# Kernel optimization log

Hardware: AMD Instinct MI355X
Metric: run time of the kernel (lower is better)

The kernel has to match this reference:

```python
import jax, jax.numpy as jnp
import numpy as np

N_SAMPLES = 2 ** 15          # 32768
STEP = 256                   # transform_step_size
WIN = 2048                   # transform/synthesis window
N_FRAMES = N_SAMPLES // STEP # 128
N_COEFFS = WIN // 2 + 1      # 1025
DILATIONS = (1, 2, 4, 8, 16, 32, 64, 1)


def hann(n):
    return 0.5 - 0.5 * jnp.cos(2.0 * jnp.pi * jnp.arange(n, dtype=jnp.float32) / n)


def transform(audio):
    # audio: (B, 1, N) -> magnitude STFT (B, 1024, 128)
    x = audio[:, 0, :]
    x = jnp.pad(x, ((0, 0), (0, WIN - STEP)))  # pad so n_frames == N_SAMPLES // STEP
    idx = np.arange(N_FRAMES)[:, None] * STEP + np.arange(WIN)[None, :]
    frames = x[:, idx] * hann(WIN)
    spec = jnp.abs(jnp.fft.rfft(frames, norm='ortho'))   # (B, F, 1025)
    return spec[..., : N_COEFFS - 1].transpose(0, 2, 1)  # (B, 1024, F)


def conv1x1(x, w, b):
    # x: (B, I, T), w: (O, I, 1), b: (O,)
    return jnp.einsum('oi,bit->bot', w[:, :, 0], x) + b[None, :, None]


def anticausal_block(x, w, b, dilation):
    # kernel_size=2 anti-causal dilated conv: looks at t and t+dilation (pad future)
    x_fut = jnp.pad(x, ((0, 0), (0, 0), (0, dilation)))[:, :, dilation:]
    y = (jnp.einsum('oi,bit->bot', w[:, :, 0], x)
         + jnp.einsum('oi,bit->bot', w[:, :, 1], x_fut)
         + b[None, :, None])
    y = jax.nn.leaky_relu(y, 0.2)
    y = y + x
    # do_norm: per-example max-norm
    y = y / (jnp.max(jnp.abs(y), axis=(1, 2), keepdims=True) + 1e-8)
    return y


def upsample_with_holes(x, desired_size):
    # zero-stuffing upsample: out[..., ::step] = x
    b, c, t = x.shape
    step = desired_size // t
    out = jnp.zeros((b, c, desired_size), x.dtype)
    return out.at[:, :, ::step].set(x)


def freq_domain_resonance(coeffs):
    # coeffs: (1, C, 1025) in [0, 1); per-frame decay = repeated spectral multiply
    c = jnp.clip(coeffs, 0.0, 0.9999)
    exps = jnp.arange(1, N_FRAMES + 1, dtype=coeffs.dtype)
    mags = c[:, :, None, :] ** exps[None, None, :, None]     # (1, C, F, 1025)
    frames = jnp.fft.irfft(mags, n=WIN) * hann(WIN)
    hop = WIN // 2
    total = hop * (N_FRAMES - 1) + WIN
    idx = np.arange(N_FRAMES)[:, None] * hop + np.arange(WIN)[None, :]
    out = jnp.zeros(frames.shape[:2] + (total,), frames.dtype)
    out = out.at[:, :, idx].add(frames)                      # overlap-add
    return out[..., :N_SAMPLES]                              # (1, C, N)


def fft_convolve(a, b):
    # circular-free conv via zero-padding to 2N, keep first N (matches repo fft_convolve)
    n = a.shape[-1]
    spec = jnp.fft.rfft(a, n=2 * n) * jnp.fft.rfft(b, n=2 * n)
    return jnp.fft.irfft(spec, n=2 * n)[..., :n]


def reference(audio, proj_in_w, proj_in_b, blocks_w, blocks_b,
              proj_sparse_w, proj_sparse_b, proj_dense_w, proj_dense_b, resonances):
    spec = transform(audio)                         # (B, 1024, 128)
    h = conv1x1(spec, proj_in_w, proj_in_b)         # (B, 32, 128)
    acc = jnp.zeros_like(h)
    for i, d in enumerate(DILATIONS):               # fixed 8-block stack
        h = anticausal_block(h, blocks_w[i], blocks_b[i], d)
        acc = acc + h
    x = conv1x1(acc, proj_sparse_w, proj_sparse_b)  # (B, 256, 128)
    sparse = jax.nn.relu(x)
    x = conv1x1(sparse, proj_dense_w, proj_dense_b) # (B, 32, 128)
    x = upsample_with_holes(x, N_SAMPLES)           # (B, 32, 32768)
    res = freq_domain_resonance(resonances)         # (1, 32, 32768), broadcast over B
    y = fft_convolve(x, res)                        # (B, 32, 32768)
    y = jnp.sum(y, axis=1, keepdims=True)           # (B, 1, 32768)
    return y, sparse


def setup_inputs() -> dict:
    key = jax.random.key(0)
    ks = jax.random.split(key, 12)
    u = lambda k, shape: jax.random.uniform(k, shape, jnp.float32, -0.05, 0.05)
    return {
        'audio': jax.random.normal(ks[0], (32, 1, N_SAMPLES), jnp.float32),
        'proj_in_w': u(ks[1], (32, 1024, 1)),
        'proj_in_b': jnp.zeros((32,), jnp.float32),
        'blocks_w': u(ks[2], (8, 32, 32, 2)),
        'blocks_b': jnp.zeros((8, 32), jnp.float32),
        'proj_sparse_w': u(ks[3], (256, 32, 1)),
        'proj_sparse_b': jnp.zeros((256,), jnp.float32),
        'proj_dense_w': u(ks[4], (32, 256, 1)),
        'proj_dense_b': jnp.zeros((32,), jnp.float32),
        'resonances': jax.random.uniform(ks[5], (1, 32, N_COEFFS), jnp.float32, 0.0, 1.0),
    }
```

## Files before the change

kernel.cpp:

```cpp
#include <hip/hip_runtime.h>

#define PI_F 3.14159265358979323846f

typedef short bf16x8 __attribute__((ext_vector_type(8)));
typedef float f32x4 __attribute__((ext_vector_type(4)));

#define MFMA16(acc, a, b) \
  acc = __builtin_amdgcn_mfma_f32_16x16x32_bf16(a, b, acc, 0, 0, 0)

#define WS_SPEC   0u
#define WS_H0     4194304u
#define WS_ACC    4325376u
#define WS_V      4456448u
#define WS_WTIN   4587520u
#define WS_WST    4620288u
#define WS_WDT    4628480u
#define WS_FRAMES 4636672u
#define WS_RES    6733824u

__device__ __forceinline__ void fft2048_stages(float2* buf, int tid) {
  for (int stage = 0; stage < 11; ++stage) {
    int half = 1 << stage;
    float base = -PI_F / (float)half;
    for (int t = tid; t < 1024; t += 256) {
      int j  = t & (half - 1);
      int i0 = ((t >> stage) << (stage + 1)) + j;
      int i1 = i0 + half;
      float s, c;
      __sincosf(base * (float)j, &s, &c);
      float2 u = buf[i0];
      float2 w = buf[i1];
      float tr = c * w.x - s * w.y;
      float ti = c * w.y + s * w.x;
      buf[i0] = make_float2(u.x + tr, u.y + ti);
      buf[i1] = make_float2(u.x - tr, u.y - ti);
    }
    __syncthreads();
  }
}

__global__ __launch_bounds__(256) void k_fft(const float* __restrict__ audio,
                                             const float* __restrict__ resin,
                                             float* __restrict__ spec,
                                             float* __restrict__ frames) {
  __shared__ float2 buf[2048];
  int blk = blockIdx.x;
  if (blk < 2048) {
    int b  = blk >> 6;
    int f0 = (blk & 63) * 2;
    for (int j = threadIdx.x; j < 2048; j += 256) {
      float h = 0.5f - 0.5f * __cosf(0.0030679615757712823f * (float)j);
      int i1 = f0 * 256 + j;
      int i2 = i1 + 256;
      float a1 = (i1 < 32768) ? audio[b * 32768 + i1] : 0.f;
      float a2 = (i2 < 32768) ? audio[b * 32768 + i2] : 0.f;
      buf[__brev((unsigned)j) >> 21] = make_float2(a1 * h, a2 * h);
    }
    __syncthreads();
    fft2048_stages(buf, threadIdx.x);
    const float scale = 0.5f * 0.022097086912079608f;
    for (int k = threadIdx.x; k < 1024; k += 256) {
      float2 zk = buf[k];
      float2 zn = buf[(2048 - k) & 2047];
      float f1r = zk.x + zn.x, f1i = zk.y - zn.y;
      float f2r = zk.y + zn.y, f2i = zk.x - zn.x;
      spec[(b * 128 + f0) * 1024 + k]     = sqrtf(f1r * f1r + f1i * f1i) * scale;
      spec[(b * 128 + f0 + 1) * 1024 + k] = sqrtf(f2r * f2r + f2i * f2i) * scale;
    }
  } else {
    int r = blk - 2048;
    int c = r >> 4;
    int g = r & 15;
    float e1 = (float)(2 * g + 1);
    for (int k = threadIdx.x; k < 2048; k += 256) {
      int kk = (k <= 1024) ? k : 2048 - k;
      float cv = resin[c * 1025 + kk];
      cv = fminf(fmaxf(cv, 0.f), 0.9999f);
      float m1 = __powf(cv, e1);
      float m2 = m1 * cv;
      buf[__brev((unsigned)k) >> 21] = make_float2(m1, m2);
    }
    __syncthreads();
    fft2048_stages(buf, threadIdx.x);
    for (int j = threadIdx.x; j < 2048; j += 256) {
      float h  = 0.5f - 0.5f * __cosf(0.0030679615757712823f * (float)j);
      float sc = h * (1.f / 2048.f);
      float2 z = buf[j];
      frames[(c * 32 + 2 * g) * 2048 + j]     = z.x * sc;
      frames[(c * 32 + 2 * g + 1) * 2048 + j] = z.y * sc;
    }
  }
}

__global__ __launch_bounds__(256) void k_prep(const float* __restrict__ Win,
                                              const float* __restrict__ Ws,
                                              const float* __restrict__ Wd,
                                              const float* __restrict__ bwIn,
                                              float* __restrict__ WT,
                                              float* __restrict__ WsT,
                                              float* __restrict__ WdT,
                                              short* __restrict__ Whg,
                                              short* __restrict__ Wlg) {
  int i = blockIdx.x * 256 + threadIdx.x;
  if (i < 32768) { int o = i >> 10, k = i & 1023; WT[k * 32 + o] = Win[i]; }
  if (i < 8192)  { int o2 = i >> 5, m = i & 31;   WsT[m * 256 + o2] = Ws[i]; }
  if (i < 8192)  { int c = i >> 8, o2 = i & 255;  WdT[o2 * 32 + c] = Wd[i]; }
  if (i < 16384) {
    int w = i & 1, m = (i >> 1) & 31, o = (i >> 6) & 31, s = i >> 11;
    float val = bwIn[i];
    unsigned bits = __float_as_uint(val);
    float rem = val - __uint_as_float(bits & 0xffff0000u);
    int row = (s * 2 + w) * 32 + o;
    Whg[row * 32 + m] = (short)(bits >> 16);
    Wlg[row * 32 + m] = (short)(__float_as_uint(rem) >> 16);
  }
}

__global__ __launch_bounds__(256) void k_proj_in(const float* __restrict__ spec,
                                                 const float* __restrict__ WT,
                                                 const float* __restrict__ bias,
                                                 float* __restrict__ h0) {
  __shared__ float specL[8][1024];
  __shared__ float red[32][8][8];
  int b  = blockIdx.x >> 4;
  int t0 = (blockIdx.x & 15) * 8;
  for (int i = threadIdx.x; i < 8192; i += 256) {
    int tt = i >> 10, k = i & 1023;
    specL[tt][k] = spec[(b * 128 + t0 + tt) * 1024 + k];
  }
  __syncthreads();
  int o = threadIdx.x & 31, p = threadIdx.x >> 5;
  float part[8] = {0.f,0.f,0.f,0.f,0.f,0.f,0.f,0.f};
  for (int i = 0; i < 128; ++i) {
    int k = p * 128 + ((i + p * 4) & 127);
    float w = WT[k * 32 + o];
#pragma unroll
    for (int tt = 0; tt < 8; ++tt) part[tt] += w * specL[tt][k];
  }
#pragma unroll
  for (int tt = 0; tt < 8; ++tt) red[o][tt][p] = part[tt];
  __syncthreads();
  int oo = threadIdx.x >> 3, tt2 = threadIdx.x & 7;
  float s = bias[oo];
#pragma unroll
  for (int p2 = 0; p2 < 8; ++p2) s += red[oo][tt2][p2];
  h0[b * 4096 + oo * 128 + t0 + tt2] = s;
}

__global__ __launch_bounds__(1024) void k_chain(const float* __restrict__ h0,
                                                const short* __restrict__ Whg,
                                                const short* __restrict__ Wlg,
                                                const float* __restrict__ bb,
                                                float* __restrict__ accout) {
  __shared__ __align__(16) short Hh[192 * 40];
  __shared__ __align__(16) short Hl[192 * 40];
  __shared__ float Hf[128 * 33];
  __shared__ float bL[256];
  __shared__ float red[16];
  int b = blockIdx.x, tid = threadIdx.x;

  for (int i = tid; i < 4096; i += 1024) {
    int t = i & 127;
    int o = i >> 7;
    float val = h0[b * 4096 + i];
    Hf[t * 33 + o] = val;
    unsigned bits = __float_as_uint(val);
    float rem = val - __uint_as_float(bits & 0xffff0000u);
    Hh[t * 40 + o] = (short)(bits >> 16);
    Hl[t * 40 + o] = (short)(__float_as_uint(rem) >> 16);
  }
  for (int i = tid; i < 64 * 40; i += 1024) {
    Hh[128 * 40 + i] = 0;
    Hl[128 * 40 + i] = 0;
  }
  if (tid < 256) bL[tid] = bb[tid];
  __syncthreads();

  int wave = tid >> 6, lane = tid & 63;
  int quad = lane >> 4, l15 = lane & 15;
  int t0 = (wave & 7) * 16, o0 = (wave >> 3) * 16;
  int tD = t0 + quad * 4;
  int oD = o0 + l15;

  const bf16x8* Hh8 = (const bf16x8*)Hh;
  const bf16x8* Hl8 = (const bf16x8*)Hl;
  const bf16x8* Wh8 = (const bf16x8*)Whg;
  const bf16x8* Wl8 = (const bf16x8*)Wlg;

  float accsum[4] = {0.f, 0.f, 0.f, 0.f};
  const int DIL[8] = {1, 2, 4, 8, 16, 32, 64, 1};

#pragma unroll
  for (int s = 0; s < 8; ++s) {
    int arow = t0 + l15;
    int frow = arow + DIL[s];
    bf16x8 Ah = Hh8[arow * 5 + quad];
    bf16x8 Al = Hl8[arow * 5 + quad];
    bf16x8 Fh = Hh8[frow * 5 + quad];
    bf16x8 Fl = Hl8[frow * 5 + quad];
    int w0row = ((s * 2 + 0) * 32 + oD) * 4 + quad;
    int w1row = ((s * 2 + 1) * 32 + oD) * 4 + quad;
    bf16x8 B0h = Wh8[w0row], B0l = Wl8[w0row];
    bf16x8 B1h = Wh8[w1row], B1l = Wl8[w1row];
    float bias = bL[s * 32 + oD];
    f32x4 acc = {bias, bias, bias, bias};
    MFMA16(acc, Ah, B0h); MFMA16(acc, Ah, B0l); MFMA16(acc, Al, B0h);
    MFMA16(acc, Fh, B1h); MFMA16(acc, Fh, B1l); MFMA16(acc, Fl, B1h);
    float hnew[4], lmax = 0.f;
#pragma unroll
    for (int r = 0; r < 4; ++r) {
      float sv = acc[r];
      sv = (sv > 0.f) ? sv : 0.2f * sv;
      sv += Hf[(tD + r) * 33 + oD];
      hnew[r] = sv;
      lmax = fmaxf(lmax, fabsf(sv));
    }
#pragma unroll
    for (int off = 32; off > 0; off >>= 1)
      lmax = fmaxf(lmax, __shfl_down(lmax, off, 64));
    if (lane == 0) red[wave] = lmax;
    __syncthreads();
    float mx = red[0];
#pragma unroll
    for (int i = 1; i < 16; ++i) mx = fmaxf(mx, red[i]);
    float nm = 1.f / (mx + 1e-8f);
#pragma unroll
    for (int r = 0; r < 4; ++r) {
      float hv = hnew[r] * nm;
      accsum[r] += hv;
      int t = tD + r;
      Hf[t * 33 + oD] = hv;
      unsigned bits = __float_as_uint(hv);
      float rem = hv - __uint_as_float(bits & 0xffff0000u);
      Hh[t * 40 + oD] = (short)(bits >> 16);
      Hl[t * 40 + oD] = (short)(__float_as_uint(rem) >> 16);
    }
    __syncthreads();
  }
#pragma unroll
  for (int r = 0; r < 4; ++r)
    accout[b * 4096 + (tD + r) * 32 + oD] = accsum[r];
}

__global__ __launch_bounds__(256) void k_sparse_dense(const float* __restrict__ acc,
                                                      const float* __restrict__ WsT,
                                                      const float* __restrict__ bs,
                                                      const float* __restrict__ WdT,
                                                      const float* __restrict__ bd,
                                                      float* __restrict__ out_sparse,
                                                      float* __restrict__ v) {
  __shared__ float accL[4][32];
  __shared__ float sL[4][256];
  __shared__ float red[8][4][32];
  int b = blockIdx.x >> 5, tq = blockIdx.x & 31;
  int t0 = tq * 4;
  int tid = threadIdx.x;
  if (tid < 128)
    accL[tid >> 5][tid & 31] = acc[b * 4096 + (t0 + (tid >> 5)) * 32 + (tid & 31)];
  __syncthreads();
  float bsv = bs[tid];
  float s0 = bsv, s1 = bsv, s2 = bsv, s3 = bsv;
  for (int m = 0; m < 32; ++m) {
    float w = WsT[m * 256 + tid];
    s0 += w * accL[0][m]; s1 += w * accL[1][m];
    s2 += w * accL[2][m]; s3 += w * accL[3][m];
  }
  s0 = fmaxf(s0, 0.f); s1 = fmaxf(s1, 0.f); s2 = fmaxf(s2, 0.f); s3 = fmaxf(s3, 0.f);
  float* os = out_sparse + b * 32768 + tid * 128 + t0;
  os[0] = s0; os[1] = s1; os[2] = s2; os[3] = s3;
  sL[0][tid] = s0; sL[1][tid] = s1; sL[2][tid] = s2; sL[3][tid] = s3;
  __syncthreads();
  int c = tid & 31, p = tid >> 5;
  float p0 = 0.f, p1 = 0.f, p2 = 0.f, p3 = 0.f;
  for (int jj = 0; jj < 32; ++jj) {
    int o2 = p * 32 + jj;
    float w = WdT[o2 * 32 + c];
    p0 += w * sL[0][o2]; p1 += w * sL[1][o2];
    p2 += w * sL[2][o2]; p3 += w * sL[3][o2];
  }
  red[p][0][c] = p0; red[p][1][c] = p1; red[p][2][c] = p2; red[p][3][c] = p3;
  __syncthreads();
  if (tid < 128) {
    int tt = tid >> 5, cc = tid & 31;
    float vv = bd[cc];
#pragma unroll
    for (int p2i = 0; p2i < 8; ++p2i) vv += red[p2i][tt][cc];
    v[b * 4096 + cc * 128 + t0 + tt] = vv;
  }
}

__global__ __launch_bounds__(256) void k_obpack(const float* __restrict__ frames,
                                                short* __restrict__ Bh,
                                                short* __restrict__ Bl) {
  int c = blockIdx.x >> 4, o = blockIdx.x & 15;
  int r = threadIdx.x;
  bf16x8 hv, lv;
#pragma unroll
  for (int j = 0; j < 8; ++j) {
    int fo = 8 * o + j;
    int g  = fo >> 2;
    int j0 = ((fo & 3) << 8) + r;
    float val = frames[(c * 32 + g) * 2048 + j0];
    if (g > 0) val += frames[(c * 32 + g - 1) * 2048 + j0 + 1024];
    unsigned bits = __float_as_uint(val);
    float rem = val - __uint_as_float(bits & 0xffff0000u);
    hv[j] = (short)(bits >> 16);
    lv[j] = (short)(__float_as_uint(rem) >> 16);
  }
  int unit = (blockIdx.x * 16 + (r >> 4)) * 16 + (r & 15);
  ((bf16x8*)Bh)[unit] = hv;
  ((bf16x8*)Bl)[unit] = lv;
}

__global__ __launch_bounds__(512, 4) void k_conv(const float* __restrict__ v,
                                                 const short* __restrict__ Bh,
                                                 const short* __restrict__ Bl,
                                                 float* __restrict__ y) {
  __shared__ __align__(16) short AH[32 * 264];
  __shared__ __align__(16) short AL[32 * 264];
  __shared__ float vwin[2][16][48];

  int xcd  = blockIdx.x & 7;
  int slot = blockIdx.x >> 3;
  int e, b;
  if      (slot < 32) { e = xcd;      b = slot; }
  else if (slot < 64) { e = xcd + 8;  b = slot - 32; }
  else                { e = (xcd < 4) ? (xcd + 16) : (xcd + 12);
                        b = (xcd < 4) ? (slot - 64) : (slot - 48); }
  int j, uc;
  if      (e < 2)  { j = 0; uc = e; }
  else if (e < 6)  { j = 1; uc = e - 2; }
  else if (e < 12) { j = 2; uc = e - 6; }
  else             { j = 3; uc = e - 12; }
  int D0 = 32 * j - 16 * uc;

  for (int i = threadIdx.x; i < 1504; i += 512) {
    int ii = i % 47;
    int r  = i / 47;
    int c  = r & 15, ph = r >> 4;
    int d  = D0 - 15 + ii;
    vwin[ph][c][ii] = (d >= 0 && d < 128)
        ? v[b * 4096 + (16 * ph + c) * 128 + d] : 0.f;
  }
  __syncthreads();

  int lane = threadIdx.x & 63, wave = threadIdx.x >> 6;
  int quad = lane >> 4, l15 = lane & 15;
  int cq   = quad >> 1;
  int og   = 2 * uc + (quad & 1);
  int nt0  = wave * 2;

  f32x4 acc00 = (f32x4)0.f, acc01 = (f32x4)0.f;
  f32x4 acc10 = (f32x4)0.f, acc11 = (f32x4)0.f;

  const bf16x8* AH8 = (const bf16x8*)AH;
  const bf16x8* AL8 = (const bf16x8*)AL;
  const bf16x8* Bh8 = (const bf16x8*)Bh;
  const bf16x8* Bl8 = (const bf16x8*)Bl;
  short2* AH2 = (short2*)AH;
  short2* AL2 = (short2*)AL;

  int abase0 = (0 * 16 + l15) * 33 + quad;
  int abase1 = (1 * 16 + l15) * 33 + quad;

  for (int p = 0; p < 2; ++p) {
    for (int i = threadIdx.x; i < 4096; i += 512) {
      int kk2 = i & 127;
      int row = i >> 7;
      int cl  = kk2 >> 3;
      int uu  = (kk2 & 7) * 2;
      int ii  = row - uu + 15;
      float v0 = vwin[p][cl][ii];
      float v1 = vwin[p][cl][ii - 1];
      unsigned w0 = __float_as_uint(v0), w1 = __float_as_uint(v1);
      float r0 = v0 - __uint_as_float(w0 & 0xffff0000u);
      float r1 = v1 - __uint_as_float(w1 & 0xffff0000u);
      int u2 = row * 132 + kk2;
      AH2[u2] = make_short2((short)(w0 >> 16), (short)(w1 >> 16));
      AL2[u2] = make_short2((short)(__float_as_uint(r0) >> 16),
                            (short)(__float_as_uint(r1) >> 16));
    }
    __syncthreads();

#pragma unroll
    for (int ks = 0; ks < 8; ++ks) {
      bf16x8 ah0 = AH8[abase0 + ks * 4];
      bf16x8 al0 = AL8[abase0 + ks * 4];
      bf16x8 ah1 = AH8[abase1 + ks * 4];
      bf16x8 al1 = AL8[abase1 + ks * 4];
      int c   = 16 * p + 2 * ks + cq;
      int bb0 = (c * 16 + og) * 256 + l15;
      bf16x8 bh0 = Bh8[bb0 + nt0 * 16];
      bf16x8 bl0 = Bl8[bb0 + nt0 * 16];
      bf16x8 bh1 = Bh8[bb0 + (nt0 + 1) * 16];
      bf16x8 bl1 = Bl8[bb0 + (nt0 + 1) * 16];
      MFMA16(acc00, ah0, bh0); MFMA16(acc00, ah0, bl0); MFMA16(acc00, al0, bh0);
      MFMA16(acc10, ah1, bh0); MFMA16(acc10, ah1, bl0); MFMA16(acc10, al1, bh0);
      MFMA16(acc01, ah0, bh1); MFMA16(acc01, ah0, bl1); MFMA16(acc01, al0, bh1);
      MFMA16(acc11, ah1, bh1); MFMA16(acc11, ah1, bl1); MFMA16(acc11, al1, bh1);
    }
    __syncthreads();
  }

  {
    float* yb0 = y + b * 32768 + (32 * j + 0 * 16 + quad * 4) * 256 + l15;
    float* yb1 = y + b * 32768 + (32 * j + 1 * 16 + quad * 4) * 256 + l15;
#pragma unroll
    for (int reg = 0; reg < 4; ++reg) {
      atomicAdd(yb0 + reg * 256 + (nt0 + 0) * 16, acc00[reg]);
      atomicAdd(yb0 + reg * 256 + (nt0 + 1) * 16, acc01[reg]);
      atomicAdd(yb1 + reg * 256 + (nt0 + 0) * 16, acc10[reg]);
      atomicAdd(yb1 + reg * 256 + (nt0 + 1) * 16, acc11[reg]);
    }
  }
}

extern "C" void kernel_launch(void* const* d_in, const int* in_sizes, int n_in,
                              void* d_out, int out_size, void* d_ws, size_t ws_size,
                              hipStream_t stream) {
  const float* audio = (const float*)d_in[0];
  const float* Win   = (const float*)d_in[1];
  const float* bin   = (const float*)d_in[2];
  const float* bw    = (const float*)d_in[3];
  const float* bb    = (const float*)d_in[4];
  const float* Ws    = (const float*)d_in[5];
  const float* bs    = (const float*)d_in[6];
  const float* Wd    = (const float*)d_in[7];
  const float* bd    = (const float*)d_in[8];
  const float* reson = (const float*)d_in[9];

  float* out = (float*)d_out;
  float* ws  = (float*)d_ws;

  float* spec   = ws + WS_SPEC;
  float* h0     = ws + WS_H0;
  float* accb   = ws + WS_ACC;
  float* vbuf   = ws + WS_V;
  float* WT     = ws + WS_WTIN;
  float* WsT    = ws + WS_WST;
  float* WdT    = ws + WS_WDT;
  float* frames = ws + WS_FRAMES;
  short* Bh = (short*)(ws + WS_RES);
  short* Bl = (short*)(ws + WS_RES + 524288u);
  short* Whg = (short*)(ws + WS_V);
  short* Wlg = (short*)(ws + WS_V + 8192u);

  hipMemsetAsync(d_out, 0, 1048576u * sizeof(float), stream);

  k_prep<<<128, 256, 0, stream>>>(Win, Ws, Wd, bw, WT, WsT, WdT, Whg, Wlg);
  k_fft<<<2560, 256, 0, stream>>>(audio, reson, spec, frames);
  k_obpack<<<512, 256, 0, stream>>>(frames, Bh, Bl);
  k_proj_in<<<512, 256, 0, stream>>>(spec, WT, bin, h0);
  k_chain<<<32, 1024, 0, stream>>>(h0, Whg, Wlg, bb, accb);
  k_sparse_dense<<<1024, 256, 0, stream>>>(accb, WsT, bs, WdT, bd, out + 1048576, vbuf);
  k_conv<<<640, 512, 0, stream>>>(vbuf, Bh, Bl, out);
}
```

Measured before the change: 189.5 us.

## Specialize early and late FFT stages, fold weight prep into FFT kernel

Rewrites the 2048-point radix-2 FFT so the first three stages use constant twiddles, the middle stages compute one sincos per thread per stage, and the last two stages reuse a single sincos through symmetry identities. This cuts the per-butterfly transcendental work. The weight-transpose and bf16-split prep kernel is merged into the FFT launch as extra blocks, which removes one kernel launch. The k_obpack definition is only moved within the file. Risks are small numerical differences from the derived twiddles and a slightly longer tail on the FFT grid.

```diff
diff --git a/kernel.cpp b/kernel.cpp
--- a/kernel.cpp
+++ b/kernel.cpp
@@ -18,33 +18,106 @@
 #define WS_FRAMES 4636672u
 #define WS_RES    6733824u
 
+#define BFLY(I0, I1, C, S)                                   \
+  { float2 u = buf[I0]; float2 w = buf[I1];                  \
+    float tr = (C) * w.x - (S) * w.y;                        \
+    float ti = (C) * w.y + (S) * w.x;                        \
+    buf[I0] = make_float2(u.x + tr, u.y + ti);               \
+    buf[I1] = make_float2(u.x - tr, u.y - ti); }
+
 __device__ __forceinline__ void fft2048_stages(float2* buf, int tid) {
-  for (int stage = 0; stage < 11; ++stage) {
+  for (int t = tid; t < 1024; t += 256) {
+    int i0 = 2 * t, i1 = i0 + 1;
+    float2 u = buf[i0], w = buf[i1];
+    buf[i0] = make_float2(u.x + w.x, u.y + w.y);
+    buf[i1] = make_float2(u.x - w.x, u.y - w.y);
+  }
+  __syncthreads();
+  for (int t = tid; t < 1024; t += 256) {
+    int j  = t & 1;
+    int i0 = ((t >> 1) << 2) + j, i1 = i0 + 2;
+    float2 u = buf[i0], w = buf[i1];
+    float tr = j ? w.y : w.x;
+    float ti = j ? -w.x : w.y;
+    buf[i0] = make_float2(u.x + tr, u.y + ti);
+    buf[i1] = make_float2(u.x - tr, u.y - ti);
+  }
+  __syncthreads();
+  for (int t = tid; t < 1024; t += 256) {
+    int j  = t & 3;
+    int i0 = ((t >> 2) << 3) + j, i1 = i0 + 4;
+    const float R = 0.7071067811865476f;
+    float c = (j == 0) ? 1.f : ((j == 1) ? R : ((j == 2) ? 0.f : -R));
+    float s = (j == 0) ? 0.f : ((j == 2) ? -1.f : -R);
+    BFLY(i0, i1, c, s);
+  }
+  __syncthreads();
+  for (int stage = 3; stage <= 8; ++stage) {
     int half = 1 << stage;
-    float base = -PI_F / (float)half;
+    int j = tid & (half - 1);
+    float s, c;
+    __sincosf(-PI_F / (float)half * (float)j, &s, &c);
     for (int t = tid; t < 1024; t += 256) {
-      int j  = t & (half - 1);
       int i0 = ((t >> stage) << (stage + 1)) + j;
       int i1 = i0 + half;
-      float s, c;
-      __sincosf(base * (float)j, &s, &c);
-      float2 u = buf[i0];
-      float2 w = buf[i1];
-      float tr = c * w.x - s * w.y;
-      float ti = c * w.y + s * w.x;
-      buf[i0] = make_float2(u.x + tr, u.y + ti);
-      buf[i1] = make_float2(u.x - tr, u.y - ti);
-    }
-    __syncthreads();
-  }
+      BFLY(i0, i1, c, s);
+    }
+    __syncthreads();
+  }
+  {
+    float s, c;
+    __sincosf(-PI_F / 512.f * (float)tid, &s, &c);
+    BFLY(tid,        tid + 512,  c, s);
+    BFLY(1024 + tid, 1536 + tid, c, s);
+    BFLY(tid + 256,  tid + 768,  s, -c);
+    BFLY(1280 + tid, 1792 + tid, s, -c);
+  }
+  __syncthreads();
+  {
+    float s0, c0;
+    __sincosf(-PI_F / 1024.f * (float)tid, &s0, &c0);
+    const float R = 0.7071067811865476f;
+    BFLY(tid,       tid + 1024, c0, s0);
+    BFLY(tid + 256, tid + 1280, R * (c0 + s0), R * (s0 - c0));
+    BFLY(tid + 512, tid + 1536, s0, -c0);
+    BFLY(tid + 768, tid + 1792, R * (s0 - c0), -R * (s0 + c0));
+  }
+  __syncthreads();
 }
 
 __global__ __launch_bounds__(256) void k_fft(const float* __restrict__ audio,
                                              const float* __restrict__ resin,
+                                             const float* __restrict__ Win,
+                                             const float* __restrict__ Ws,
+                                             const float* __restrict__ Wd,
+                                             const float* __restrict__ bwIn,
                                              float* __restrict__ spec,
-                                             float* __restrict__ frames) {
+                                             float* __restrict__ frames,
+                                             float* __restrict__ WT,
+                                             float* __restrict__ WsT,
+                                             float* __restrict__ WdT,
+                                             short* __restrict__ Whg,
+                                             short* __restrict__ Wlg) {
   __shared__ float2 buf[2048];
   int blk = blockIdx.x;
+
+  if (blk >= 2560) {
+    int i = (blk - 2560) * 256 + threadIdx.x;
+    if (i < 32768) { int o = i >> 10, k = i & 1023; WT[k * 32 + o] = Win[i]; }
+    if (i < 8192)  { int o2 = i >> 5, m = i & 31;   WsT[m * 256 + o2] = Ws[i]; }
+    if (i < 8192)  { int c = i >> 8, o2 = i & 255;  WdT[o2 * 32 + c] = Wd[i]; }
+    if (i < 16384) {
+      int w = i & 1, m = (i >> 1) & 31, o = (i >> 6) & 31, s = i >> 11;
+      float val = bwIn[i];
+      unsigned bits = __float_as_uint(val);
+      float rem = val - __uint_as_float(bits & 0xffff0000u);
+      int row = (s * 2 + w) * 32 + o;
+      Whg[row * 32 + m] = (short)(bits >> 16);
+      Wlg[row * 32 + m] = (short)(__float_as_uint(rem) >> 16);
+    }
+    return;
+  }
+
   if (blk < 2048) {
     int b  = blk >> 6;
     int f0 = (blk & 63) * 2;
@@ -92,30 +165,6 @@
   }
 }
 
-__global__ __launch_bounds__(256) void k_prep(const float* __restrict__ Win,
-                                              const float* __restrict__ Ws,
-                                              const float* __restrict__ Wd,
-                                              const float* __restrict__ bwIn,
-                                              float* __restrict__ WT,
-                                              float* __restrict__ WsT,
-                                              float* __restrict__ WdT,
-                                              short* __restrict__ Whg,
-                                              short* __restrict__ Wlg) {
-  int i = blockIdx.x * 256 + threadIdx.x;
-  if (i < 32768) { int o = i >> 10, k = i & 1023; WT[k * 32 + o] = Win[i]; }
-  if (i < 8192)  { int o2 = i >> 5, m = i & 31;   WsT[m * 256 + o2] = Ws[i]; }
-  if (i < 8192)  { int c = i >> 8, o2 = i & 255;  WdT[o2 * 32 + c] = Wd[i]; }
-  if (i < 16384) {
-    int w = i & 1, m = (i >> 1) & 31, o = (i >> 6) & 31, s = i >> 11;
-    float val = bwIn[i];
-    unsigned bits = __float_as_uint(val);
-    float rem = val - __uint_as_float(bits & 0xffff0000u);
-    int row = (s * 2 + w) * 32 + o;
-    Whg[row * 32 + m] = (short)(bits >> 16);
-    Wlg[row * 32 + m] = (short)(__float_as_uint(rem) >> 16);
-  }
-}
-
 __global__ __launch_bounds__(256) void k_proj_in(const float* __restrict__ spec,
                                                  const float* __restrict__ WT,
                                                  const float* __restrict__ bias,
@@ -145,6 +194,29 @@
 #pragma unroll
   for (int p2 = 0; p2 < 8; ++p2) s += red[oo][tt2][p2];
   h0[b * 4096 + oo * 128 + t0 + tt2] = s;
+}
+
+__global__ __launch_bounds__(256) void k_obpack(const float* __restrict__ frames,
+                                                short* __restrict__ Bh,
+                                                short* __restrict__ Bl) {
+  int c = blockIdx.x >> 4, o = blockIdx.x & 15;
+  int r = threadIdx.x;
+  bf16x8 hv, lv;
+#pragma unroll
+  for (int j = 0; j < 8; ++j) {
+    int fo = 8 * o + j;
+    int g  = fo >> 2;
+    int j0 = ((fo & 3) << 8) + r;
+    float val = frames[(c * 32 + g) * 2048 + j0];
+    if (g > 0) val += frames[(c * 32 + g - 1) * 2048 + j0 + 1024];
+    unsigned bits = __float_as_uint(val);
+    float rem = val - __uint_as_float(bits & 0xffff0000u);
+    hv[j] = (short)(bits >> 16);
+    lv[j] = (short)(__float_as_uint(rem) >> 16);
+  }
+  int unit = (blockIdx.x * 16 + (r >> 4)) * 16 + (r & 15);
+  ((bf16x8*)Bh)[unit] = hv;
+  ((bf16x8*)Bl)[unit] = lv;
 }
 
 __global__ __launch_bounds__(1024) void k_chain(const float* __restrict__ h0,
@@ -289,29 +361,6 @@
   }
 }
 
-__global__ __launch_bounds__(256) void k_obpack(const float* __restrict__ frames,
-                                                short* __restrict__ Bh,
-                                                short* __restrict__ Bl) {
-  int c = blockIdx.x >> 4, o = blockIdx.x & 15;
-  int r = threadIdx.x;
-  bf16x8 hv, lv;
-#pragma unroll
-  for (int j = 0; j < 8; ++j) {
-    int fo = 8 * o + j;
-    int g  = fo >> 2;
-    int j0 = ((fo & 3) << 8) + r;
-    float val = frames[(c * 32 + g) * 2048 + j0];
-    if (g > 0) val += frames[(c * 32 + g - 1) * 2048 + j0 + 1024];
-    unsigned bits = __float_as_uint(val);
-    float rem = val - __uint_as_float(bits & 0xffff0000u);
-    hv[j] = (short)(bits >> 16);
-    lv[j] = (short)(__float_as_uint(rem) >> 16);
-  }
-  int unit = (blockIdx.x * 16 + (r >> 4)) * 16 + (r & 15);
-  ((bf16x8*)Bh)[unit] = hv;
-  ((bf16x8*)Bl)[unit] = lv;
-}
-
 __global__ __launch_bounds__(512, 4) void k_conv(const float* __restrict__ v,
                                                  const short* __restrict__ Bh,
                                                  const short* __restrict__ Bl,
@@ -447,8 +496,8 @@
 
   hipMemsetAsync(d_out, 0, 1048576u * sizeof(float), stream);
 
-  k_prep<<<128, 256, 0, stream>>>(Win, Ws, Wd, bw, WT, WsT, WdT, Whg, Wlg);
-  k_fft<<<2560, 256, 0, stream>>>(audio, reson, spec, frames);
+  k_fft<<<2688, 256, 0, stream>>>(audio, reson, Win, Ws, Wd, bw,
+                                  spec, frames, WT, WsT, WdT, Whg, Wlg);
   k_obpack<<<512, 256, 0, stream>>>(frames, Bh, Bl);
   k_proj_in<<<512, 256, 0, stream>>>(spec, WT, bin, h0);
   k_chain<<<32, 1024, 0, stream>>>(h0, Whg, Wlg, bb, accb);
```

After: 188.6 us. No clear change (-0.5%).
